# Kernel optimization log

Measured on AMD Instinct MI355X. Metric: run time of the kernel, lower is better.

The kernel has to match this reference:

```python
import jax, jax.numpy as jnp
import numpy as np

B, N, F = 32, 2048, 32  # batch, num_elements, feature_size = num_classes + num_geometry


def setup_inputs() -> dict:
    key = jax.random.key(0)
    ks = jax.random.split(key, 5)
    s = 1.0 / np.sqrt(F)
    return {
        "x": jax.random.normal(ks[0], (B, N, F), dtype=jnp.float32),
        "w_psi": jax.random.normal(ks[1], (F, F), dtype=jnp.float32) * s,
        "b_psi": jnp.zeros((F,), dtype=jnp.float32),
        "w_phi": jax.random.normal(ks[2], (F, F), dtype=jnp.float32) * s,
        "b_phi": jnp.zeros((F,), dtype=jnp.float32),
        "w_u": jax.random.normal(ks[3], (F, F), dtype=jnp.float32) * s,
        "b_u": jnp.zeros((F,), dtype=jnp.float32),
        "w_r": jax.random.normal(ks[4], (F, F), dtype=jnp.float32) * s,
    }


def reference(x, w_psi, b_psi, w_phi, b_phi, w_u, b_u, w_r):
    # psi/phi: per-element linear embeddings; u: relu unary representation
    psi = x @ w_psi + b_psi                      # [B,N,F]
    phi = x @ w_phi + b_phi                      # [B,N,F]
    u = jax.nn.relu(x @ w_u + b_u)               # [B,N,F]
    # H(i,j) = psi_i . phi_j  -> all-pairs scalar affinities
    scores = jnp.einsum('bif,bjf->bij', psi, phi)          # [B,N,N]
    # sum_j H(i,j) * u_j, then remove the j==i self term
    att = jnp.einsum('bij,bjf->bif', scores, u)            # [B,N,F]
    diag = jnp.einsum('bif,bif->bi', psi, phi)             # H(i,i)
    att = att - diag[..., None] * u
    # residual: W_r * (attention / N) + f_i
    return (att / N) @ w_r + x
```

## Files before the change

### kernel.cpp

```cpp
#include <hip/hip_runtime.h>


namespace {
constexpr int kF = 32;
constexpr int kN = 2048;
constexpr int kB = 32;
}

typedef __attribute__((ext_vector_type(8))) short bf16x8;
typedef __attribute__((ext_vector_type(16))) float f32x16;

union BF8 { bf16x8 v; int i[4]; };

__device__ inline int pk2(float lo, float hi) {
    union { float f; unsigned int u; } a, b;
    a.f = lo; b.f = hi;
    return (int)((a.u + 0x8000u) >> 16) | (int)((b.u + 0x8000u) & 0xFFFF0000u);
}

__device__ inline void load_wfrags(const float* __restrict__ W, int ld, int col, int h,
                                   bf16x8& f0, bf16x8& f1) {
    BF8 a, b;
#pragma unroll
    for (int q = 0; q < 4; ++q)
        a.i[q] = pk2(W[(8 * h + 2 * q) * ld + col], W[(8 * h + 2 * q + 1) * ld + col]);
#pragma unroll
    for (int q = 0; q < 4; ++q)
        b.i[q] = pk2(W[(16 + 8 * h + 2 * q) * ld + col], W[(16 + 8 * h + 2 * q + 1) * ld + col]);
    f0 = a.v; f1 = b.v;
}

__device__ inline void load_xfrags(const float* __restrict__ xr, int h,
                                   bf16x8& f0, bf16x8& f1) {
    float4 a = *(const float4*)(xr + 8 * h);
    float4 b = *(const float4*)(xr + 8 * h + 4);
    float4 c = *(const float4*)(xr + 16 + 8 * h);
    float4 d = *(const float4*)(xr + 16 + 8 * h + 4);
    BF8 u0, u1;
    u0.i[0] = pk2(a.x, a.y); u0.i[1] = pk2(a.z, a.w);
    u0.i[2] = pk2(b.x, b.y); u0.i[3] = pk2(b.z, b.w);
    u1.i[0] = pk2(c.x, c.y); u1.i[1] = pk2(c.z, c.w);
    u1.i[2] = pk2(d.x, d.y); u1.i[3] = pk2(d.z, d.w);
    f0 = u0.v; f1 = u1.v;
}

__device__ inline void c_to_kfrags(const f32x16& v, int h, bf16x8& f0, bf16x8& f1) {
    int p[8], t[8];
#pragma unroll
    for (int q = 0; q < 8; ++q) p[q] = pk2(v[2 * q], v[2 * q + 1]);
#pragma unroll
    for (int q = 0; q < 8; ++q) t[q] = __shfl_xor(p[q], 32, 64);
    BF8 a, b;
    a.i[0] = h ? t[2] : p[0];
    a.i[1] = h ? t[3] : p[1];
    a.i[2] = h ? p[2] : t[0];
    a.i[3] = h ? p[3] : t[1];
    b.i[0] = h ? t[6] : p[4];
    b.i[1] = h ? t[7] : p[5];
    b.i[2] = h ? p[6] : t[4];
    b.i[3] = h ? p[7] : t[5];
    f0 = a.v; f1 = b.v;
}

__device__ inline f32x16 zero16() {
    f32x16 z;
#pragma unroll
    for (int i = 0; i < 16; ++i) z[i] = 0.f;
    return z;
}

#define MFMA(A, B, C) __builtin_amdgcn_mfma_f32_32x32x16_bf16(A, B, C, 0, 0, 0)

__global__ __launch_bounds__(256, 2) void k_partial_m(
    const float* __restrict__ x,
    const float* __restrict__ w_phi, const float* __restrict__ b_phi,
    const float* __restrict__ w_u,   const float* __restrict__ b_u,
    float* __restrict__ part)
{
    __shared__ float red_s[4][64 * 20];

    const int tid = threadIdx.x;
    const int lane = tid & 63;
    const int w = tid >> 6;
    const int col = lane & 31;
    const int h = lane >> 5;
    const int blk = blockIdx.x;
    const int row0 = blk * 128 + w * 32;

    bf16x8 ax0, ax1;
    load_xfrags(x + (size_t)(row0 + col) * kF, h, ax0, ax1);

    f32x16 phiC = zero16(), uC = zero16();
    {
        bf16x8 bp0, bp1;
        load_wfrags(w_phi, kF, col, h, bp0, bp1);
        phiC = MFMA(ax0, bp0, phiC); phiC = MFMA(ax1, bp1, phiC);
    }
    {
        bf16x8 bu0, bu1;
        load_wfrags(w_u, kF, col, h, bu0, bu1);
        uC = MFMA(ax0, bu0, uC); uC = MFMA(ax1, bu1, uC);
    }

    const float bphi = b_phi[col];
    const float bu = b_u[col];
#pragma unroll
    for (int r = 0; r < 16; ++r) {
        phiC[r] += bphi;
        uC[r] = fmaxf(uC[r] + bu, 0.f);
    }

    bf16x8 ap0, ap1, fu0, fu1;
    c_to_kfrags(phiC, h, ap0, ap1);
    c_to_kfrags(uC, h, fu0, fu1);
    f32x16 macc = zero16();
    macc = MFMA(ap0, fu0, macc);
    macc = MFMA(ap1, fu1, macc);

    float* rs = red_s[w] + lane * 20;
#pragma unroll
    for (int q = 0; q < 4; ++q)
        *(float4*)(rs + 4 * q) = make_float4(macc[4 * q], macc[4 * q + 1],
                                             macc[4 * q + 2], macc[4 * q + 3]);
    __syncthreads();

    const int lp = tid >> 2;
    const int q = tid & 3;
    float4 s = make_float4(0.f, 0.f, 0.f, 0.f);
#pragma unroll
    for (int ww = 0; ww < 4; ++ww) {
        float4 v = *(const float4*)(red_s[ww] + lp * 20 + 4 * q);
        s.x += v.x; s.y += v.y; s.z += v.z; s.w += v.w;
    }
    *(float4*)(part + (size_t)blk * 1024 + tid * 4) = s;
}

__global__ __launch_bounds__(256, 2) void k_relation(
    const float* __restrict__ x,
    const float* __restrict__ w_psi, const float* __restrict__ b_psi,
    const float* __restrict__ w_phi, const float* __restrict__ b_phi,
    const float* __restrict__ w_u,   const float* __restrict__ b_u,
    const float* __restrict__ w_r,
    const float* __restrict__ part,
    float* __restrict__ out)
{
    __shared__ float t_s[4][32 * 36];
    __shared__ float m_s[kF * 33];

    const int tid = threadIdx.x;
    const int lane = tid & 63;
    const int w = tid >> 6;
    const int col = lane & 31;
    const int h = lane >> 5;
    const int blk = blockIdx.x;
    const int row0 = blk * 128 + w * 32;
    const int b = blk >> 4;

    {
        const float* pb = part + (size_t)(b * 16) * 1024 + tid * 4;
        float4 ms = make_float4(0.f, 0.f, 0.f, 0.f);
#pragma unroll
        for (int p = 0; p < 16; ++p) {
            float4 v = *(const float4*)(pb + p * 1024);
            ms.x += v.x; ms.y += v.y; ms.z += v.z; ms.w += v.w;
        }
        const int lp = tid >> 2;
        const int q = tid & 3;
        const int g = lp & 31;
        const int f0 = 8 * q + 4 * (lp >> 5);
        m_s[(f0 + 0) * 33 + g] = ms.x;
        m_s[(f0 + 1) * 33 + g] = ms.y;
        m_s[(f0 + 2) * 33 + g] = ms.z;
        m_s[(f0 + 3) * 33 + g] = ms.w;
    }

    bf16x8 ax0, ax1;
    load_xfrags(x + (size_t)(row0 + col) * kF, h, ax0, ax1);

    f32x16 psiT = zero16();
    {
        bf16x8 a0, a1;
        load_wfrags(w_psi, kF, col, h, a0, a1);
        psiT = MFMA(a0, ax0, psiT); psiT = MFMA(a1, ax1, psiT);
    }
    float d;
    {
        f32x16 phiT = zero16();
        bf16x8 a0, a1;
        load_wfrags(w_phi, kF, col, h, a0, a1);
        phiT = MFMA(a0, ax0, phiT); phiT = MFMA(a1, ax1, phiT);
        d = 0.f;
#pragma unroll
        for (int r = 0; r < 16; ++r) {
            const int gg = (r & 3) + 8 * (r >> 2);
            psiT[r] += h ? b_psi[gg + 4] : b_psi[gg];
            const float phv = phiT[r] + (h ? b_phi[gg + 4] : b_phi[gg]);
            d += psiT[r] * phv;
        }
        d += __shfl_xor(d, 32, 64);
    }
    f32x16 uT = zero16();
    {
        bf16x8 a0, a1;
        load_wfrags(w_u, kF, col, h, a0, a1);
        uT = MFMA(a0, ax0, uT); uT = MFMA(a1, ax1, uT);
#pragma unroll
        for (int r = 0; r < 16; ++r) {
            const int gg = (r & 3) + 8 * (r >> 2);
            uT[r] = fmaxf(uT[r] + (h ? b_u[gg + 4] : b_u[gg]), 0.f);
        }
    }

    f32x16 attT = zero16();
    {
        bf16x8 bps0, bps1;
        c_to_kfrags(psiT, h, bps0, bps1);
        __syncthreads();
        bf16x8 am0, am1;
        load_wfrags(m_s, 33, col, h, am0, am1);
        attT = MFMA(am0, bps0, attT);
        attT = MFMA(am1, bps1, attT);
    }

    const float inv_n = 1.0f / (float)kN;
#pragma unroll
    for (int r = 0; r < 16; ++r) attT[r] = (attT[r] - d * uT[r]) * inv_n;

    f32x16 corrT = zero16();
    {
        bf16x8 bt0, bt1;
        c_to_kfrags(attT, h, bt0, bt1);
        bf16x8 a0, a1;
        load_wfrags(w_r, kF, col, h, a0, a1);
        corrT = MFMA(a0, bt0, corrT);
        corrT = MFMA(a1, bt1, corrT);
    }

    float* ts = t_s[w];
#pragma unroll
    for (int qq = 0; qq < 4; ++qq)
        *(float4*)(ts + col * 36 + 8 * qq + 4 * h) =
            make_float4(corrT[4 * qq], corrT[4 * qq + 1],
                        corrT[4 * qq + 2], corrT[4 * qq + 3]);

    const size_t gbase = (size_t)row0 * kF;
#pragma unroll
    for (int qq = 0; qq < 4; ++qq) {
        const int idx = qq * 256 + lane * 4;
        const int el = idx >> 5;
        const int cc = idx & 31;
        float4 cv = *(const float4*)(ts + el * 36 + cc);
        float4 xv = *(const float4*)(x + gbase + idx);
        *(float4*)(out + gbase + idx) =
            make_float4(xv.x + cv.x, xv.y + cv.y, xv.z + cv.z, xv.w + cv.w);
    }
}

extern "C" void kernel_launch(void* const* d_in, const int* in_sizes, int n_in,
                              void* d_out, int out_size, void* d_ws, size_t ws_size,
                              hipStream_t stream) {
    const float* x     = (const float*)d_in[0];
    const float* w_psi = (const float*)d_in[1];
    const float* b_psi = (const float*)d_in[2];
    const float* w_phi = (const float*)d_in[3];
    const float* b_phi = (const float*)d_in[4];
    const float* w_u   = (const float*)d_in[5];
    const float* b_u   = (const float*)d_in[6];
    const float* w_r   = (const float*)d_in[7];
    float* out = (float*)d_out;
    float* part = (float*)d_ws;

    k_partial_m<<<dim3(512), 256, 0, stream>>>(x, w_phi, b_phi, w_u, b_u, part);
    k_relation<<<dim3(512), 256, 0, stream>>>(x, w_psi, b_psi, w_phi, b_phi,
                                              w_u, b_u, w_r, part, out);
}
```

Baseline: 83.05 us.

## Fuse both kernels into one cooperative kernel with grid-wide sync

Measured after the change: 84.34 us. No clear change (+1.5%).

```diff
diff --git a/kernel.cpp b/kernel.cpp
--- a/kernel.cpp
+++ b/kernel.cpp
@@ -1,4 +1,7 @@
 #include <hip/hip_runtime.h>
+#include <hip/hip_cooperative_groups.h>
+
+namespace cg = cooperative_groups;
 
 
 namespace {
@@ -71,6 +74,169 @@
 
 #define MFMA(A, B, C) __builtin_amdgcn_mfma_f32_32x32x16_bf16(A, B, C, 0, 0, 0)
 
+__global__ __launch_bounds__(256, 2) void k_fused(
+    const float* __restrict__ x,
+    const float* __restrict__ w_psi, const float* __restrict__ b_psi,
+    const float* __restrict__ w_phi, const float* __restrict__ b_phi,
+    const float* __restrict__ w_u,   const float* __restrict__ b_u,
+    const float* __restrict__ w_r,
+    float* __restrict__ part,
+    float* __restrict__ out)
+{
+    __shared__ float sh[4][64 * 20];
+    __shared__ float m_s[kF * 33];
+
+    const int tid = threadIdx.x;
+    const int lane = tid & 63;
+    const int w = tid >> 6;
+    const int col = lane & 31;
+    const int h = lane >> 5;
+    const int blk = blockIdx.x;
+    const int row0 = blk * 128 + w * 32;
+    const int b = blk >> 4;
+
+    bf16x8 ax0, ax1;
+    load_xfrags(x + (size_t)(row0 + col) * kF, h, ax0, ax1);
+    bf16x8 bp0, bp1, bu0, bu1;
+    load_wfrags(w_phi, kF, col, h, bp0, bp1);
+    load_wfrags(w_u,   kF, col, h, bu0, bu1);
+
+    f32x16 phiC = zero16(), uC = zero16();
+    phiC = MFMA(ax0, bp0, phiC); phiC = MFMA(ax1, bp1, phiC);
+    uC   = MFMA(ax0, bu0, uC);   uC   = MFMA(ax1, bu1, uC);
+
+    const float bphi = b_phi[col];
+    const float bub = b_u[col];
+#pragma unroll
+    for (int r = 0; r < 16; ++r) {
+        phiC[r] += bphi;
+        uC[r] = fmaxf(uC[r] + bub, 0.f);
+    }
+
+    {
+        bf16x8 ap0, ap1, fu0, fu1;
+        c_to_kfrags(phiC, h, ap0, ap1);
+        c_to_kfrags(uC, h, fu0, fu1);
+        f32x16 macc = zero16();
+        macc = MFMA(ap0, fu0, macc);
+        macc = MFMA(ap1, fu1, macc);
+
+        float* rs = sh[w] + lane * 20;
+#pragma unroll
+        for (int q = 0; q < 4; ++q)
+            *(float4*)(rs + 4 * q) = make_float4(macc[4 * q], macc[4 * q + 1],
+                                                 macc[4 * q + 2], macc[4 * q + 3]);
+    }
+    __syncthreads();
+    {
+        const int lp = tid >> 2;
+        const int q = tid & 3;
+        float4 s = make_float4(0.f, 0.f, 0.f, 0.f);
+#pragma unroll
+        for (int ww = 0; ww < 4; ++ww) {
+            float4 v = *(const float4*)(sh[ww] + lp * 20 + 4 * q);
+            s.x += v.x; s.y += v.y; s.z += v.z; s.w += v.w;
+        }
+        *(float4*)(part + (size_t)blk * 1024 + tid * 4) = s;
+    }
+
+    __threadfence();
+    cg::this_grid().sync();
+    __threadfence();
+
+    {
+        const float* pb = part + (size_t)(b * 16) * 1024 + tid * 4;
+        float4 ms = make_float4(0.f, 0.f, 0.f, 0.f);
+#pragma unroll
+        for (int p = 0; p < 16; ++p) {
+            float4 v = *(const float4*)(pb + p * 1024);
+            ms.x += v.x; ms.y += v.y; ms.z += v.z; ms.w += v.w;
+        }
+        const int lp = tid >> 2;
+        const int q = tid & 3;
+        const int g = lp & 31;
+        const int f0 = 8 * q + 4 * (lp >> 5);
+        m_s[(f0 + 0) * 33 + g] = ms.x;
+        m_s[(f0 + 1) * 33 + g] = ms.y;
+        m_s[(f0 + 2) * 33 + g] = ms.z;
+        m_s[(f0 + 3) * 33 + g] = ms.w;
+    }
+
+    f32x16 psiT = zero16();
+    {
+        bf16x8 a0, a1;
+        load_wfrags(w_psi, kF, col, h, a0, a1);
+        psiT = MFMA(a0, ax0, psiT); psiT = MFMA(a1, ax1, psiT);
+    }
+    float d;
+    {
+        f32x16 phiT = zero16();
+        phiT = MFMA(bp0, ax0, phiT); phiT = MFMA(bp1, ax1, phiT);
+        d = 0.f;
+#pragma unroll
+        for (int r = 0; r < 16; ++r) {
+            const int gg = (r & 3) + 8 * (r >> 2);
+            psiT[r] += h ? b_psi[gg + 4] : b_psi[gg];
+            const float phv = phiT[r] + (h ? b_phi[gg + 4] : b_phi[gg]);
+            d += psiT[r] * phv;
+        }
+        d += __shfl_xor(d, 32, 64);
+    }
+    f32x16 uT = zero16();
+    {
+        uT = MFMA(bu0, ax0, uT); uT = MFMA(bu1, ax1, uT);
+#pragma unroll
+        for (int r = 0; r < 16; ++r) {
+            const int gg = (r & 3) + 8 * (r >> 2);
+            uT[r] = fmaxf(uT[r] + (h ? b_u[gg + 4] : b_u[gg]), 0.f);
+        }
+    }
+
+    f32x16 attT = zero16();
+    {
+        bf16x8 bps0, bps1;
+        c_to_kfrags(psiT, h, bps0, bps1);
+        __syncthreads();
+        bf16x8 am0, am1;
+        load_wfrags(m_s, 33, col, h, am0, am1);
+        attT = MFMA(am0, bps0, attT);
+        attT = MFMA(am1, bps1, attT);
+    }
+
+    const float inv_n = 1.0f / (float)kN;
+#pragma unroll
+    for (int r = 0; r < 16; ++r) attT[r] = (attT[r] - d * uT[r]) * inv_n;
+
+    f32x16 corrT = zero16();
+    {
+        bf16x8 bt0, bt1;
+        c_to_kfrags(attT, h, bt0, bt1);
+        bf16x8 a0, a1;
+        load_wfrags(w_r, kF, col, h, a0, a1);
+        corrT = MFMA(a0, bt0, corrT);
+        corrT = MFMA(a1, bt1, corrT);
+    }
+
+    float* ts = sh[w];
+#pragma unroll
+    for (int qq = 0; qq < 4; ++qq)
+        *(float4*)(ts + col * 36 + 8 * qq + 4 * h) =
+            make_float4(corrT[4 * qq], corrT[4 * qq + 1],
+                        corrT[4 * qq + 2], corrT[4 * qq + 3]);
+
+    const size_t gbase = (size_t)row0 * kF;
+#pragma unroll
+    for (int qq = 0; qq < 4; ++qq) {
+        const int idx = qq * 256 + lane * 4;
+        const int el = idx >> 5;
+        const int cc = idx & 31;
+        float4 cv = *(const float4*)(ts + el * 36 + cc);
+        float4 xv = *(const float4*)(x + gbase + idx);
+        *(float4*)(out + gbase + idx) =
+            make_float4(xv.x + cv.x, xv.y + cv.y, xv.z + cv.z, xv.w + cv.w);
+    }
+}
+
 __global__ __launch_bounds__(256, 2) void k_partial_m(
     const float* __restrict__ x,
     const float* __restrict__ w_phi, const float* __restrict__ b_phi,
@@ -103,11 +269,11 @@
     }
 
     const float bphi = b_phi[col];
-    const float bu = b_u[col];
+    const float bub = b_u[col];
 #pragma unroll
     for (int r = 0; r < 16; ++r) {
         phiC[r] += bphi;
-        uC[r] = fmaxf(uC[r] + bu, 0.f);
+        uC[r] = fmaxf(uC[r] + bub, 0.f);
     }
 
     bf16x8 ap0, ap1, fu0, fu1;
@@ -270,7 +436,20 @@
     float* out = (float*)d_out;
     float* part = (float*)d_ws;
 
-    k_partial_m<<<dim3(512), 256, 0, stream>>>(x, w_phi, b_phi, w_u, b_u, part);
-    k_relation<<<dim3(512), 256, 0, stream>>>(x, w_psi, b_psi, w_phi, b_phi,
-                                              w_u, b_u, w_r, part, out);
-}
+    int occ = 0;
+    hipError_t qerr = hipOccupancyMaxActiveBlocksPerMultiprocessor(
+        &occ, k_fused, 256, 0);
+
+    if (qerr == hipSuccess && occ >= 2) {
+        void* args[] = {
+            (void*)&x, (void*)&w_psi, (void*)&b_psi, (void*)&w_phi, (void*)&b_phi,
+            (void*)&w_u, (void*)&b_u, (void*)&w_r, (void*)&part, (void*)&out,
+        };
+        hipLaunchCooperativeKernel((void*)k_fused, dim3(512), dim3(256),
+                                   args, 0, stream);
+    } else {
+        k_partial_m<<<dim3(512), 256, 0, stream>>>(x, w_phi, b_phi, w_u, b_u, part);
+        k_relation<<<dim3(512), 256, 0, stream>>>(x, w_psi, b_psi, w_phi, b_phi,
+                                                  w_u, b_u, w_r, part, out);
+    }
+}
```
